# Optimization experiments

Hardware: AMD Instinct MI355X
Metric: run time of the kernel (lower is better)

## Reference

```python
import jax, jax.numpy as jnp
import numpy as np


def setup_inputs() -> dict:
    key = jax.random.key(0)
    k1, k2, k3, k4 = jax.random.split(key, 4)
    B, N, F_in, F_out = 8, 2048, 256, 256
    v = jax.random.normal(k1, (B, N, F_in), dtype=jnp.float32)
    adj = jax.random.uniform(k2, (B, N, N), dtype=jnp.float32)  # pairwise distances
    # torch Linear weights: [out_features, in_features], scaled like kaiming-uniform-ish
    W1 = jax.random.normal(k3, (F_out, F_in), dtype=jnp.float32) * (1.0 / np.sqrt(F_in))
    W2 = jax.random.normal(k4, (F_out, F_in), dtype=jnp.float32) * (1.0 / np.sqrt(F_in))
    return {"v": v, "adj": adj, "W1": W1, "W2": W2}


def reference(v, adj, W1, W2):
    D = 100.0
    # Linear projections (no bias): [B,N,F_in] @ [F_in,F_out]
    c1 = jnp.einsum("bnf,of->bno", v, W1)
    c2 = jnp.einsum("bnf,of->bno", v, W2)
    # Pairwise scores: [B,N,N]
    s = jnp.einsum("bno,bmo->bnm", c1, c2)
    c = jax.nn.sigmoid(s) * D + 1e-05
    c = 1.0 / (2.0 * c * c)
    norm_adj = jnp.exp(-(adj * adj * c))
    return (v, norm_adj)
```

## Files before the change

kernel.cpp:

```cpp
#include <hip/hip_runtime.h>


typedef _Float16 half8_t __attribute__((ext_vector_type(8)));
typedef _Float16 half4_t __attribute__((ext_vector_type(4)));
typedef float floatx4 __attribute__((ext_vector_type(4)));

#define LDSS 72
#define PS   132

__global__ void prep_kernel(const floatx4* __restrict__ v4,
                            floatx4* __restrict__ out4,
                            half4_t* __restrict__ vf4) {
    int idx = blockIdx.x * 256 + threadIdx.x;
    floatx4 t = v4[idx];
    out4[idx] = t;
    half4_t h;
    h[0] = (_Float16)t[0]; h[1] = (_Float16)t[1];
    h[2] = (_Float16)t[2]; h[3] = (_Float16)t[3];
    vf4[idx] = h;
}

__global__ void mt_kernel(const float* __restrict__ W1,
                          const float* __restrict__ W2,
                          _Float16* __restrict__ Mt) {
    __shared__ float w2col[256];
    const int j = blockIdx.x;
    const int i = threadIdx.x;
    w2col[i] = W2[i * 256 + j];
    __syncthreads();
    float acc = 0.f;
    #pragma unroll 8
    for (int o = 0; o < 256; ++o)
        acc += w2col[o] * W1[o * 256 + i];
    Mt[j * 256 + i] = (_Float16)acc;
}

template<int MODE>
__global__ __launch_bounds__(256, 4)
void gemm_kernel(const _Float16* __restrict__ A, const _Float16* __restrict__ Bm,
                 size_t a_bstride, size_t b_bstride,
                 _Float16* __restrict__ Uout,
                 const float* __restrict__ adj, float* __restrict__ out) {
    __shared__ _Float16 smem[2 * 128 * LDSS];
    _Float16* As = smem;
    _Float16* Bs = smem + 128 * LDSS;

    const int tid  = threadIdx.x;
    const int lane = tid & 63;
    const int wid  = tid >> 6;
    const int wm   = wid >> 1;
    const int wn   = wid & 1;
    const int quad = lane >> 4;
    const int l16  = lane & 15;

    const int m0 = blockIdx.x * 128;
    const int n0 = blockIdx.y * 128;
    const int batch = blockIdx.z;

    const _Float16* Ab = A  + (size_t)batch * a_bstride;
    const _Float16* Bb = Bm + (size_t)batch * b_bstride;

    floatx4 acc[4][4];
    #pragma unroll
    for (int i = 0; i < 4; ++i)
        #pragma unroll
        for (int j = 0; j < 4; ++j)
            acc[i][j] = (floatx4){0.f, 0.f, 0.f, 0.f};

    const int rrow = tid >> 3;
    const int ch8  = (tid & 7) * 8;

    for (int kc = 0; kc < 256; kc += 64) {
        __syncthreads();
        #pragma unroll
        for (int r = 0; r < 4; ++r) {
            int row = r * 32 + rrow;
            uint4 va = *(const uint4*)(Ab + (((size_t)(m0 + row)) << 8) + kc + ch8);
            uint4 vb = *(const uint4*)(Bb + (((size_t)(n0 + row)) << 8) + kc + ch8);
            *(uint4*)(&As[row * LDSS + ch8]) = va;
            *(uint4*)(&Bs[row * LDSS + ch8]) = vb;
        }
        __syncthreads();
        #pragma unroll
        for (int ks = 0; ks < 2; ++ks) {
            const int kof = ks * 32 + quad * 8;
            half8_t mf[4], nf[4];
            #pragma unroll
            for (int t = 0; t < 4; ++t) {
                mf[t] = *(const half8_t*)(&As[(wm * 64 + t * 16 + l16) * LDSS + kof]);
                nf[t] = *(const half8_t*)(&Bs[(wn * 64 + t * 16 + l16) * LDSS + kof]);
            }
            #pragma unroll
            for (int i = 0; i < 4; ++i)
                #pragma unroll
                for (int j = 0; j < 4; ++j)
                    acc[i][j] = __builtin_amdgcn_mfma_f32_16x16x32_f16(
                        nf[i], mf[j], acc[i][j], 0, 0, 0);
        }
    }

    if (MODE == 0) {
        #pragma unroll
        for (int j = 0; j < 4; ++j) {
            int m = m0 + wm * 64 + j * 16 + l16;
            #pragma unroll
            for (int i = 0; i < 4; ++i) {
                int n = wn * 64 + i * 16 + quad * 4;
                half4_t h;
                #pragma unroll
                for (int r = 0; r < 4; ++r) h[r] = (_Float16)acc[i][j][r];
                *(half4_t*)(Uout + (size_t)m * 256 + n0 + n) = h;
            }
        }
    } else {
        __syncthreads();
        _Float16* Ps = smem;
        #pragma unroll
        for (int j = 0; j < 4; ++j) {
            int ml = wm * 64 + j * 16 + l16;
            #pragma unroll
            for (int i = 0; i < 4; ++i) {
                int nl = wn * 64 + i * 16 + quad * 4;
                half4_t h;
                #pragma unroll
                for (int r = 0; r < 4; ++r) {
                    float s = acc[i][j][r];
                    float p = 100.0f / (1.0f + __expf(-s)) + 1e-5f;
                    h[r] = (_Float16)p;
                }
                *(half4_t*)(&Ps[ml * PS + nl]) = h;
            }
        }
        __syncthreads();

        const int srow = tid >> 5;
        const int scol = (tid & 31) * 4;
        const size_t gbase = (size_t)batch * 2048 * 2048
                           + (size_t)m0 * 2048 + n0 + scol;
        #pragma unroll 4
        for (int pass = 0; pass < 16; ++pass) {
            int r = pass * 8 + srow;
            size_t g = gbase + (size_t)r * 2048;
            floatx4 a = *(const floatx4*)(adj + g);
            half4_t ph = *(const half4_t*)(&Ps[r * PS + scol]);
            floatx4 o;
            #pragma unroll
            for (int e = 0; e < 4; ++e) {
                float ip = __builtin_amdgcn_rcpf((float)ph[e]);
                float q = a[e] * ip;
                o[e] = __expf(-0.5f * q * q);
            }
            __builtin_nontemporal_store(o, (floatx4*)(out + g));
        }
    }
}

extern "C" void kernel_launch(void* const* d_in, const int* in_sizes, int n_in,
                              void* d_out, int out_size, void* d_ws, size_t ws_size,
                              hipStream_t stream) {
    const float* v   = (const float*)d_in[0];
    const float* adj = (const float*)d_in[1];
    const float* W1  = (const float*)d_in[2];
    const float* W2  = (const float*)d_in[3];

    float* out_v   = (float*)d_out;
    float* out_adj = (float*)d_out + (size_t)8 * 2048 * 256;

    char* ws = (char*)d_ws;
    _Float16* vf = (_Float16*)ws;
    _Float16* uf = (_Float16*)(ws + ((size_t)8 << 20));
    _Float16* Mt = (_Float16*)(ws + ((size_t)16 << 20));

    prep_kernel<<<4096, 256, 0, stream>>>((const floatx4*)v, (floatx4*)out_v, (half4_t*)vf);
    mt_kernel<<<256, 256, 0, stream>>>(W1, W2, Mt);
    gemm_kernel<0><<<dim3(128, 2, 1), 256, 0, stream>>>(
        vf, Mt, 0, 0, uf, nullptr, nullptr);
    gemm_kernel<1><<<dim3(16, 16, 8), 256, 0, stream>>>(
        uf, vf, (size_t)2048 * 256, (size_t)2048 * 256, nullptr, adj, out_adj);
}
```

Before: 311.0 us.

## Split adjacency exp epilogue out of GEMM into separate streaming kernel

The score GEMM now writes the sigmoid-scaled matrix as fp16 to workspace instead of computing the Gaussian of adj inline. A new grid-stride streaming kernel reads adj and the fp16 intermediate and writes the final output with nontemporal loads and stores. The intent is to decouple the bandwidth-heavy elementwise pass from the MFMA kernel so each can run at its own best occupancy. The cost is an extra 64MB write and read of the intermediate. The k-loop is also unrolled and its first barrier removed.

Measured after the change: 333.3 us. 1.07x slower.

```diff
diff --git a/kernel.cpp b/kernel.cpp
--- a/kernel.cpp
+++ b/kernel.cpp
@@ -39,8 +39,7 @@
 __global__ __launch_bounds__(256, 4)
 void gemm_kernel(const _Float16* __restrict__ A, const _Float16* __restrict__ Bm,
                  size_t a_bstride, size_t b_bstride,
-                 _Float16* __restrict__ Uout,
-                 const float* __restrict__ adj, float* __restrict__ out) {
+                 _Float16* __restrict__ Out) {
     __shared__ _Float16 smem[2 * 128 * LDSS];
     _Float16* As = smem;
     _Float16* Bs = smem + 128 * LDSS;
@@ -52,6 +51,8 @@
     const int wn   = wid & 1;
     const int quad = lane >> 4;
     const int l16  = lane & 15;
+    const int rrow = tid >> 3;
+    const int ch8  = (tid & 7) * 8;
 
     const int m0 = blockIdx.x * 128;
     const int n0 = blockIdx.y * 128;
@@ -67,11 +68,9 @@
         for (int j = 0; j < 4; ++j)
             acc[i][j] = (floatx4){0.f, 0.f, 0.f, 0.f};
 
-    const int rrow = tid >> 3;
-    const int ch8  = (tid & 7) * 8;
-
+    #pragma unroll
     for (int kc = 0; kc < 256; kc += 64) {
-        __syncthreads();
+        if (kc) __syncthreads();
         #pragma unroll
         for (int r = 0; r < 4; ++r) {
             int row = r * 32 + rrow;
@@ -109,7 +108,7 @@
                 half4_t h;
                 #pragma unroll
                 for (int r = 0; r < 4; ++r) h[r] = (_Float16)acc[i][j][r];
-                *(half4_t*)(Uout + (size_t)m * 256 + n0 + n) = h;
+                *(half4_t*)(Out + (size_t)m * 256 + n0 + n) = h;
             }
         }
     } else {
@@ -133,25 +132,37 @@
         }
         __syncthreads();
 
+        _Float16* Pb = Out + (size_t)batch * 2048 * 2048;
         const int srow = tid >> 5;
         const int scol = (tid & 31) * 4;
-        const size_t gbase = (size_t)batch * 2048 * 2048
-                           + (size_t)m0 * 2048 + n0 + scol;
         #pragma unroll 4
         for (int pass = 0; pass < 16; ++pass) {
             int r = pass * 8 + srow;
-            size_t g = gbase + (size_t)r * 2048;
-            floatx4 a = *(const floatx4*)(adj + g);
             half4_t ph = *(const half4_t*)(&Ps[r * PS + scol]);
-            floatx4 o;
-            #pragma unroll
-            for (int e = 0; e < 4; ++e) {
-                float ip = __builtin_amdgcn_rcpf((float)ph[e]);
-                float q = a[e] * ip;
-                o[e] = __expf(-0.5f * q * q);
-            }
-            __builtin_nontemporal_store(o, (floatx4*)(out + g));
+            *(half4_t*)(Pb + (size_t)(m0 + r) * 2048 + n0 + scol) = ph;
         }
+    }
+}
+
+__global__ __launch_bounds__(256)
+void stream_kernel(const floatx4* __restrict__ adj4,
+                   const half4_t* __restrict__ p4,
+                   floatx4* __restrict__ out4) {
+    const size_t base = (size_t)blockIdx.x * 256 + threadIdx.x;
+    const size_t stride = (size_t)2048 * 256;
+    #pragma unroll 4
+    for (int it = 0; it < 16; ++it) {
+        size_t g = base + (size_t)it * stride;
+        floatx4 a = __builtin_nontemporal_load(adj4 + g);
+        half4_t ph = p4[g];
+        floatx4 o;
+        #pragma unroll
+        for (int e = 0; e < 4; ++e) {
+            float ip = __builtin_amdgcn_rcpf((float)ph[e]);
+            float q = a[e] * ip;
+            o[e] = __expf(-0.5f * q * q);
+        }
+        __builtin_nontemporal_store(o, out4 + g);
     }
 }
 
@@ -170,11 +181,14 @@
     _Float16* vf = (_Float16*)ws;
     _Float16* uf = (_Float16*)(ws + ((size_t)8 << 20));
     _Float16* Mt = (_Float16*)(ws + ((size_t)16 << 20));
+    _Float16* pf = (_Float16*)(ws + ((size_t)17 << 20));
 
     prep_kernel<<<4096, 256, 0, stream>>>((const floatx4*)v, (floatx4*)out_v, (half4_t*)vf);
     mt_kernel<<<256, 256, 0, stream>>>(W1, W2, Mt);
     gemm_kernel<0><<<dim3(128, 2, 1), 256, 0, stream>>>(
-        vf, Mt, 0, 0, uf, nullptr, nullptr);
+        vf, Mt, 0, 0, uf);
     gemm_kernel<1><<<dim3(16, 16, 8), 256, 0, stream>>>(
-        uf, vf, (size_t)2048 * 256, (size_t)2048 * 256, nullptr, adj, out_adj);
+        uf, vf, (size_t)2048 * 256, (size_t)2048 * 256, pf);
+    stream_kernel<<<2048, 256, 0, stream>>>(
+        (const floatx4*)adj, (const half4_t*)pf, (floatx4*)out_adj);
 }
```
